# Performance work log

Measured on AMD Instinct MI355X. Metric: run time of the kernel, lower is better.

Reference implementation:

```python
import jax, jax.numpy as jnp
import numpy as np

N = 50000      # nodes per type
E = 800000     # edges per relation
D = 128        # input feature dim
H = 128        # hidden_channels


def setup_inputs() -> dict:
    key = jax.random.key(0)
    ks = jax.random.split(key, 20)
    f = lambda k, shp: jax.random.normal(k, shp, dtype=jnp.float32) * 0.05
    inp = {
        "x_ligand": jax.random.normal(ks[0], (N, D), dtype=jnp.float32),
        "x_protein": jax.random.normal(ks[1], (N, D), dtype=jnp.float32),
        "ei_lp": jax.random.randint(ks[2], (2, E), 0, N, dtype=jnp.int64),
        "ei_pp": jax.random.randint(ks[3], (2, E), 0, N, dtype=jnp.int64),
        "ei_ll": jax.random.randint(ks[4], (2, E), 0, N, dtype=jnp.int64),
        "Wl_lp": f(ks[5], (D, H)), "bl_lp": f(ks[6], (H,)), "Wr_lp": f(ks[7], (D, H)),
        "Wl_pp": f(ks[8], (D, H)), "bl_pp": f(ks[9], (H,)), "Wr_pp": f(ks[10], (D, H)),
        "Wl_ll": f(ks[11], (D, H)), "bl_ll": f(ks[12], (H,)), "Wr_ll": f(ks[13], (D, H)),
        "W_out": f(ks[14], (H, 1)), "b_out": f(ks[15], (1,)),
    }
    return inp


def _sage(x_src, x_dst, edge_index, Wl, bl, Wr):
    # PyG SAGEConv: mean-aggregate neighbor (src) features onto dst, then
    # out = lin_l(agg) + lin_r(x_dst)  (lin_l has bias, lin_r does not)
    src, dst = edge_index[0], edge_index[1]
    n_dst = x_dst.shape[0]
    msgs = x_src[src]                                      # [E, D] gather
    s = jax.ops.segment_sum(msgs, dst, num_segments=n_dst) # [N_dst, D]
    cnt = jax.ops.segment_sum(jnp.ones((edge_index.shape[1],), x_src.dtype),
                              dst, num_segments=n_dst)     # [N_dst]
    agg = s / jnp.maximum(cnt, 1.0)[:, None]               # mean, 0 if isolated
    return agg @ Wl + bl + x_dst @ Wr


def reference(x_ligand, x_protein, ei_lp, ei_pp, ei_ll,
              Wl_lp, bl_lp, Wr_lp, Wl_pp, bl_pp, Wr_pp,
              Wl_ll, bl_ll, Wr_ll, W_out, b_out):
    # HeteroConv: sum contributions per destination node type
    protein_out = (_sage(x_ligand, x_protein, ei_lp, Wl_lp, bl_lp, Wr_lp)
                   + _sage(x_protein, x_protein, ei_pp, Wl_pp, bl_pp, Wr_pp))
    ligand_out = _sage(x_ligand, x_ligand, ei_ll, Wl_ll, bl_ll, Wr_ll)
    # relu per node type; only ligand is used downstream
    lig = jax.nn.relu(ligand_out).mean(axis=0)             # [H]
    _ = jax.nn.relu(protein_out)                           # computed in original
    return lig @ W_out + b_out                             # [1]
```

## Files before the change

### kernel.cpp

```cpp
#include <hip/hip_runtime.h>
#include <hip/hip_bf16.h>

#define DIM 128
#define EPB 4096
#define NRBIN 1024
#define RCAP 1280

typedef __attribute__((ext_vector_type(8))) short bf16x8;
typedef __attribute__((ext_vector_type(4))) float f32x4;
typedef __attribute__((ext_vector_type(4))) short short4v;
typedef __attribute__((ext_vector_type(4))) int int4v;

__device__ inline unsigned short f2bf(float f) {
  union { float f; unsigned u; } v; v.f = f;
  return (unsigned short)((v.u + 0x7FFFu + ((v.u >> 16) & 1u)) >> 16);
}
__device__ inline float lo_f(unsigned u) {
  union { unsigned u; float f; } v; v.u = u << 16; return v.f;
}
__device__ inline float hi_f(unsigned u) {
  union { unsigned u; float f; } v; v.u = u & 0xFFFF0000u; return v.f;
}

__global__ __launch_bounds__(256) void prep_kernel(
    const float* __restrict__ x, short* __restrict__ A,
    const float* __restrict__ Wl, const float* __restrict__ Wr,
    short* __restrict__ Bpack, int nnodes, int mpad, int xb) {
  const int bid = blockIdx.x;
  if (bid < xb) {
    int t = bid * 256 + threadIdx.x;
    int node = t >> 5;
    if (node >= mpad) return;
    int c = (t & 31) * 4;
    short4v o = (short4v){0, 0, 0, 0};
    if (node < nnodes) {
      float4 v = *reinterpret_cast<const float4*>(x + (size_t)node * DIM + c);
      o.x = (short)f2bf(v.x); o.y = (short)f2bf(v.y);
      o.z = (short)f2bf(v.z); o.w = (short)f2bf(v.w);
    }
    *reinterpret_cast<short4v*>(A + (size_t)node * 256 + 128 + c) = o;
  } else {
    int t = (bid - xb) * 256 + threadIdx.x;
    if (t >= 4096) return;
    int lane = t & 63, nt = (t >> 6) & 7, ks = t >> 9;
    int c = nt * 16 + (lane & 15);
    int kb = ks * 32 + ((lane >> 4) << 3);
    bf16x8 o;
#pragma unroll
    for (int j = 0; j < 8; ++j) {
      int k = kb + j;
      float v = (k < DIM) ? Wl[k * DIM + c] : Wr[(k - DIM) * DIM + c];
      o[j] = (short)f2bf(v);
    }
    reinterpret_cast<bf16x8*>(Bpack)[(ks * 8 + nt) * 64 + lane] = o;
  }
}

__global__ __launch_bounds__(256) void partition_kernel(
    const int* __restrict__ ei, unsigned* __restrict__ chunkbuf,
    int* __restrict__ startsT, int* __restrict__ countsT, int E) {
  __shared__ unsigned uns[EPB];
  __shared__ unsigned srt[EPB];
  __shared__ int lhist[NRBIN];
  __shared__ int lstart[NRBIN];
  __shared__ int tsum[256];
  const int tid = threadIdx.x;
  const int chunk = blockIdx.x;
  const int base = chunk * EPB;
  const int count = min(EPB, E - base);

#pragma unroll
  for (int r = 0; r < NRBIN / 256; ++r) lhist[tid + 256 * r] = 0;
  __syncthreads();

  for (int r = 0; r < EPB / 1024; ++r) {
    int i = r * 1024 + tid * 4;
    if (i + 3 < count) {
      int4 s4 = *reinterpret_cast<const int4*>(ei + base + i);
      int4 d4 = *reinterpret_cast<const int4*>(ei + E + base + i);
      int ss[4] = {s4.x, s4.y, s4.z, s4.w};
      int dd[4] = {d4.x, d4.y, d4.z, d4.w};
#pragma unroll
      for (int k = 0; k < 4; ++k) {
        unsigned reg = (unsigned)dd[k] >> 6;
        uns[i + k] = (reg << 22) | ((unsigned)(dd[k] & 63) << 16) | (unsigned)ss[k];
        atomicAdd(&lhist[reg], 1);
      }
    } else {
      for (int k = 0; k < 4; ++k) {
        if (i + k < count) {
          int s = ei[base + i + k], d = ei[E + base + i + k];
          unsigned reg = (unsigned)d >> 6;
          uns[i + k] = (reg << 22) | ((unsigned)(d & 63) << 16) | (unsigned)s;
          atomicAdd(&lhist[reg], 1);
        }
      }
    }
  }
  __syncthreads();

  int h0 = lhist[tid * 4], h1 = lhist[tid * 4 + 1];
  int h2 = lhist[tid * 4 + 2], h3 = lhist[tid * 4 + 3];
  int local = h0 + h1 + h2 + h3;
  tsum[tid] = local;
  __syncthreads();
  for (int o = 1; o < 256; o <<= 1) {
    int t = (tid >= o) ? tsum[tid - o] : 0;
    __syncthreads();
    tsum[tid] += t;
    __syncthreads();
  }
  int tb = tsum[tid] - local;
  lstart[tid * 4]     = tb;
  lstart[tid * 4 + 1] = tb + h0;
  lstart[tid * 4 + 2] = tb + h0 + h1;
  lstart[tid * 4 + 3] = tb + h0 + h1 + h2;
  lhist[tid * 4] = 0; lhist[tid * 4 + 1] = 0;
  lhist[tid * 4 + 2] = 0; lhist[tid * 4 + 3] = 0;
  __syncthreads();

  for (int i = tid; i < count; i += 256) {
    unsigned e = uns[i];
    unsigned reg = e >> 22;
    int pos = lstart[reg] + atomicAdd(&lhist[reg], 1);
    srt[pos] = e;
  }
  __syncthreads();

  for (int r = 0; r < EPB / 1024; ++r) {
    int i = r * 1024 + tid * 4;
    if (i + 3 < count) {
      int4v v = {(int)srt[i], (int)srt[i + 1], (int)srt[i + 2], (int)srt[i + 3]};
      *reinterpret_cast<int4v*>(chunkbuf + (size_t)chunk * EPB + i) = v;
    } else {
      for (int k = 0; k < 4; ++k)
        if (i + k < count) chunkbuf[(size_t)chunk * EPB + i + k] = srt[i + k];
    }
  }
  for (int r = tid; r < NRBIN; r += 256) {
    startsT[(size_t)chunk * NRBIN + r] = lstart[r];
    countsT[(size_t)chunk * NRBIN + r] = lhist[r];
  }
}

__global__ __launch_bounds__(256) void compact_kernel(
    const unsigned* __restrict__ chunkbuf, const int* __restrict__ startsT,
    const int* __restrict__ countsT, int nchunk, unsigned* __restrict__ csr,
    int* __restrict__ cnt, int* __restrict__ off) {
  __shared__ unsigned raw[RCAP];
  __shared__ unsigned srt[RCAP];
  __shared__ int h[64];
  __shared__ int start[64];
  __shared__ int tsum[256];
  const int region = blockIdx.x;
  const int tid = threadIdx.x;

  int cn = 0, st = 0;
  if (tid < nchunk) {
    cn = countsT[(size_t)tid * NRBIN + region];
    st = startsT[(size_t)tid * NRBIN + region];
  }
  tsum[tid] = cn;
  __syncthreads();
  for (int o = 1; o < 256; o <<= 1) {
    int t = (tid >= o) ? tsum[tid - o] : 0;
    __syncthreads();
    tsum[tid] += t;
    __syncthreads();
  }
  const int pfx = tsum[tid] - cn;
  int total = min(tsum[255], RCAP);

  const unsigned* src = chunkbuf + (size_t)tid * EPB + st;
  for (int j = 0; j < cn && pfx + j < RCAP; ++j) raw[pfx + j] = src[j];
  if (tid < 64) h[tid] = 0;
  __syncthreads();

  for (int i = tid; i < total; i += 256) atomicAdd(&h[(raw[i] >> 16) & 63], 1);
  __syncthreads();
  if (tid == 0) {
    int s = 0;
    for (int i = 0; i < 64; ++i) { start[i] = s; s += h[i]; }
  }
  __syncthreads();
  if (tid < 64) {
    int node = region * 64 + tid;
    cnt[node] = h[tid];
    off[node] = region * RCAP + start[tid];
    h[tid] = 0;
  }
  __syncthreads();
  for (int i = tid; i < total; i += 256) {
    unsigned e = raw[i];
    int d = (e >> 16) & 63;
    int pos = start[d] + atomicAdd(&h[d], 1);
    srt[pos] = e & 0xFFFFu;
  }
  __syncthreads();
  for (int i = tid; i < total; i += 256) csr[(size_t)region * RCAP + i] = srt[i];
}

__global__ __launch_bounds__(256) void agg_kernel(
    const int* __restrict__ cnt, const int* __restrict__ off,
    const unsigned* __restrict__ bucket, short* __restrict__ A,
    int nnodes, int mpad) {
  const int wid = (blockIdx.x * 256 + threadIdx.x) >> 6;
  const int lane = threadIdx.x & 63;
  if (wid >= mpad) return;
  unsigned* dst = reinterpret_cast<unsigned*>(A + (size_t)wid * 256) + lane;
  if (wid >= nnodes) { *dst = 0u; return; }
  const int deg  = __builtin_amdgcn_readfirstlane(cnt[wid]);
  const int base = __builtin_amdgcn_readfirstlane(off[wid]);
  const unsigned* xs = reinterpret_cast<const unsigned*>(A) + 64 + lane;

  unsigned ent = (lane < deg) ? bucket[base + lane] : 0u;
  const int dcap = min(deg, 64);

  float l0 = 0.f, h0 = 0.f, l1 = 0.f, h1 = 0.f;
  int j = 0;
  for (; j + 7 < dcap; j += 8) {
    unsigned u[8];
#pragma unroll
    for (int k = 0; k < 8; ++k) {
      int s = __builtin_amdgcn_readlane((int)ent, j + k);
      u[k] = xs[(size_t)s * 128];
    }
#pragma unroll
    for (int k = 0; k < 8; ++k) {
      if (k & 1) { l1 += lo_f(u[k]); h1 += hi_f(u[k]); }
      else       { l0 += lo_f(u[k]); h0 += hi_f(u[k]); }
    }
  }
  for (; j < dcap; ++j) {
    int s = __builtin_amdgcn_readlane((int)ent, j);
    unsigned u0 = xs[(size_t)s * 128];
    l0 += lo_f(u0); h0 += hi_f(u0);
  }
  for (; j < deg; ++j) {
    int s = __builtin_amdgcn_readfirstlane((int)bucket[base + j]);
    unsigned u0 = xs[(size_t)s * 128];
    l0 += lo_f(u0); h0 += hi_f(u0);
  }
  const float r = 1.0f / fmaxf((float)deg, 1.0f);
  const float av = (l0 + l1) * r;
  const float bv = (h0 + h1) * r;
  *dst = (unsigned)f2bf(av) | ((unsigned)f2bf(bv) << 16);
}

__global__ __launch_bounds__(256) void mfma_kernel(
    const short* __restrict__ A, const short* __restrict__ Bpack,
    const float* __restrict__ bl, float* __restrict__ partial, int nnodes) {
  __shared__ short a_lds[64 * 256];
  const int tid = threadIdx.x;
  const int wave = tid >> 6, lane = tid & 63;
  const int mt = blockIdx.x;
  const size_t abase = (size_t)mt * 64 * 256;

#pragma unroll
  for (int r = 0; r < 8; ++r) {
    int i = tid + 256 * r;
    int row = i >> 5, kc = i & 31;
    bf16x8 v = *reinterpret_cast<const bf16x8*>(A + abase + row * 256 + kc * 8);
    int byte = (row * 512 + kc * 16) ^ ((row & 7) << 4);
    *reinterpret_cast<bf16x8*>(reinterpret_cast<char*>(a_lds) + byte) = v;
  }
  __syncthreads();

  f32x4 acc[8];
#pragma unroll
  for (int nt = 0; nt < 8; ++nt) acc[nt] = (f32x4){0.f, 0.f, 0.f, 0.f};

  const int arow = wave * 16 + (lane & 15);
  const int kgrp = lane >> 4;
  const bf16x8* Bp = reinterpret_cast<const bf16x8*>(Bpack);

#pragma unroll
  for (int ks = 0; ks < 8; ++ks) {
    int byte = (arow * 512 + (ks * 32 + kgrp * 8) * 2) ^ ((arow & 7) << 4);
    bf16x8 a = *reinterpret_cast<const bf16x8*>(reinterpret_cast<char*>(a_lds) + byte);
#pragma unroll
    for (int nt = 0; nt < 8; ++nt) {
      bf16x8 b = Bp[(ks * 8 + nt) * 64 + lane];
      acc[nt] = __builtin_amdgcn_mfma_f32_16x16x32_bf16(a, b, acc[nt], 0, 0, 0);
    }
  }

  const int col16 = lane & 15;
  const int rowbase = mt * 64 + wave * 16 + kgrp * 4;
#pragma unroll
  for (int nt = 0; nt < 8; ++nt) {
    const int c = nt * 16 + col16;
    const float bb = bl[c];
    float s = 0.f;
#pragma unroll
    for (int rg = 0; rg < 4; ++rg) {
      float v = fmaxf(acc[nt][rg] + bb, 0.f);
      s += (rowbase + rg < nnodes) ? v : 0.f;
    }
    s += __shfl_xor(s, 16);
    s += __shfl_xor(s, 32);
    if (kgrp == 0) partial[((size_t)mt * 4 + wave) * DIM + c] = s;
  }
}

__global__ __launch_bounds__(256) void red1_kernel(
    const float* __restrict__ partial, int nrows, float* __restrict__ red) {
  __shared__ float tmp[128];
  const int c = threadIdx.x & 127;
  const int half = threadIdx.x >> 7;
  const int chunk = (nrows + 127) / 128;
  const int r0 = blockIdx.x * chunk;
  const int r1 = min(r0 + chunk, nrows);
  float s = 0.f;
  for (int r = r0 + half; r < r1; r += 2) s += partial[(size_t)r * DIM + c];
  if (half) tmp[c] = s;
  __syncthreads();
  if (!half) red[(size_t)blockIdx.x * DIM + c] = s + tmp[c];
}

__global__ __launch_bounds__(256) void red2_kernel(
    const float* __restrict__ red, const float* __restrict__ Wout,
    const float* __restrict__ bout, float* __restrict__ out, int nnodes) {
  __shared__ float tmp[128];
  __shared__ float prod[128];
  const int c = threadIdx.x & 127;
  const int half = threadIdx.x >> 7;
  float s = 0.f;
  for (int r = half; r < 128; r += 2) s += red[(size_t)r * DIM + c];
  if (half) tmp[c] = s;
  __syncthreads();
  if (!half) prod[c] = (s + tmp[c]) * Wout[c];
  __syncthreads();
  if (threadIdx.x == 0) {
    float v = 0.f;
    for (int i = 0; i < 128; ++i) v += prod[i];
    out[0] = v / (float)nnodes + bout[0];
  }
}

extern "C" void kernel_launch(void* const* d_in, const int* in_sizes, int n_in,
                              void* d_out, int out_size, void* d_ws, size_t ws_size,
                              hipStream_t stream) {
  const float* x    = (const float*)d_in[0];
  const int*   ei   = (const int*)d_in[4];
  const float* Wl   = (const float*)d_in[11];
  const float* bl   = (const float*)d_in[12];
  const float* Wr   = (const float*)d_in[13];
  const float* Wout = (const float*)d_in[14];
  const float* bout = (const float*)d_in[15];

  const int nnodes = in_sizes[0] / DIM;
  const int E = in_sizes[4] / 2;
  const int mtiles = (nnodes + 63) / 64;
  const int mpad = mtiles * 64;
  const int nchunk = (E + EPB - 1) / EPB;

  unsigned* chunkbuf = (unsigned*)d_ws;
  int*      startsT  = (int*)(chunkbuf + (size_t)nchunk * EPB);
  int*      countsT  = startsT + (size_t)nchunk * NRBIN;
  unsigned* csr      = (unsigned*)(countsT + (size_t)nchunk * NRBIN);
  int*      cnt      = (int*)(csr + (size_t)mtiles * RCAP);
  int*      off      = cnt + mpad;
  short*    A        = (short*)(off + mpad);
  short*    Bpack    = A + (size_t)mpad * 256;
  float*    red      = (float*)(Bpack + 32768);
  float*    partial  = (float*)chunkbuf;

  const int xb = mpad / 8;
  prep_kernel<<<xb + 16, 256, 0, stream>>>(x, A, Wl, Wr, Bpack, nnodes, mpad, xb);

  partition_kernel<<<nchunk, 256, 0, stream>>>(ei, chunkbuf, startsT, countsT, E);

  compact_kernel<<<mtiles, 256, 0, stream>>>(chunkbuf, startsT, countsT, nchunk,
                                             csr, cnt, off);

  agg_kernel<<<(mpad + 3) / 4, 256, 0, stream>>>(cnt, off, csr, A, nnodes, mpad);

  mfma_kernel<<<mtiles, 256, 0, stream>>>(A, Bpack, bl, partial, nnodes);

  red1_kernel<<<128, 256, 0, stream>>>(partial, mtiles * 4, red);
  red2_kernel<<<1, 256, 0, stream>>>(red, Wout, bout, (float*)d_out, nnodes);
}
```

Before: 95.15 us.

## Fuse prep and partition kernels; unroll aggregation gather by 16

Merges the bf16 conversion/weight-packing kernel into the edge partition kernel as extra blocks, removing one launch and letting both run concurrently. The aggregation kernel gets a 16-wide unrolled gather loop to keep more loads in flight, plus a launch-bounds occupancy hint. The trade-off is that prep blocks now carry the partition kernel's large shared-memory allocation, which may limit how many of them fit on a CU at once.

```diff
diff --git a/kernel.cpp b/kernel.cpp
--- a/kernel.cpp
+++ b/kernel.cpp
@@ -22,50 +22,52 @@
   union { unsigned u; float f; } v; v.u = u & 0xFFFF0000u; return v.f;
 }
 
-__global__ __launch_bounds__(256) void prep_kernel(
+__global__ __launch_bounds__(256) void prep_part_kernel(
+    const int* __restrict__ ei, unsigned* __restrict__ chunkbuf,
+    int* __restrict__ startsT, int* __restrict__ countsT, int E, int nchunk,
     const float* __restrict__ x, short* __restrict__ A,
     const float* __restrict__ Wl, const float* __restrict__ Wr,
     short* __restrict__ Bpack, int nnodes, int mpad, int xb) {
-  const int bid = blockIdx.x;
-  if (bid < xb) {
-    int t = bid * 256 + threadIdx.x;
-    int node = t >> 5;
-    if (node >= mpad) return;
-    int c = (t & 31) * 4;
-    short4v o = (short4v){0, 0, 0, 0};
-    if (node < nnodes) {
-      float4 v = *reinterpret_cast<const float4*>(x + (size_t)node * DIM + c);
-      o.x = (short)f2bf(v.x); o.y = (short)f2bf(v.y);
-      o.z = (short)f2bf(v.z); o.w = (short)f2bf(v.w);
-    }
-    *reinterpret_cast<short4v*>(A + (size_t)node * 256 + 128 + c) = o;
-  } else {
-    int t = (bid - xb) * 256 + threadIdx.x;
-    if (t >= 4096) return;
-    int lane = t & 63, nt = (t >> 6) & 7, ks = t >> 9;
-    int c = nt * 16 + (lane & 15);
-    int kb = ks * 32 + ((lane >> 4) << 3);
-    bf16x8 o;
-#pragma unroll
-    for (int j = 0; j < 8; ++j) {
-      int k = kb + j;
-      float v = (k < DIM) ? Wl[k * DIM + c] : Wr[(k - DIM) * DIM + c];
-      o[j] = (short)f2bf(v);
-    }
-    reinterpret_cast<bf16x8*>(Bpack)[(ks * 8 + nt) * 64 + lane] = o;
-  }
-}
-
-__global__ __launch_bounds__(256) void partition_kernel(
-    const int* __restrict__ ei, unsigned* __restrict__ chunkbuf,
-    int* __restrict__ startsT, int* __restrict__ countsT, int E) {
   __shared__ unsigned uns[EPB];
   __shared__ unsigned srt[EPB];
   __shared__ int lhist[NRBIN];
   __shared__ int lstart[NRBIN];
   __shared__ int tsum[256];
   const int tid = threadIdx.x;
-  const int chunk = blockIdx.x;
+  const int bid = blockIdx.x;
+
+  if (bid >= nchunk) {
+    if (bid < nchunk + xb) {
+      int t = (bid - nchunk) * 256 + tid;
+      int node = t >> 5;
+      if (node >= mpad) return;
+      int c = (t & 31) * 4;
+      short4v o = (short4v){0, 0, 0, 0};
+      if (node < nnodes) {
+        float4 v = *reinterpret_cast<const float4*>(x + (size_t)node * DIM + c);
+        o.x = (short)f2bf(v.x); o.y = (short)f2bf(v.y);
+        o.z = (short)f2bf(v.z); o.w = (short)f2bf(v.w);
+      }
+      *reinterpret_cast<short4v*>(A + (size_t)node * 256 + 128 + c) = o;
+    } else {
+      int t = (bid - nchunk - xb) * 256 + tid;
+      if (t >= 4096) return;
+      int lane = t & 63, nt = (t >> 6) & 7, ks = t >> 9;
+      int c = nt * 16 + (lane & 15);
+      int kb = ks * 32 + ((lane >> 4) << 3);
+      bf16x8 o;
+#pragma unroll
+      for (int j = 0; j < 8; ++j) {
+        int k = kb + j;
+        float v = (k < DIM) ? Wl[k * DIM + c] : Wr[(k - DIM) * DIM + c];
+        o[j] = (short)f2bf(v);
+      }
+      reinterpret_cast<bf16x8*>(Bpack)[(ks * 8 + nt) * 64 + lane] = o;
+    }
+    return;
+  }
+
+  const int chunk = bid;
   const int base = chunk * EPB;
   const int count = min(EPB, E - base);
 
@@ -200,7 +202,7 @@
   for (int i = tid; i < total; i += 256) csr[(size_t)region * RCAP + i] = srt[i];
 }
 
-__global__ __launch_bounds__(256) void agg_kernel(
+__global__ __launch_bounds__(256, 4) void agg_kernel(
     const int* __restrict__ cnt, const int* __restrict__ off,
     const unsigned* __restrict__ bucket, short* __restrict__ A,
     int nnodes, int mpad) {
@@ -218,6 +220,19 @@
 
   float l0 = 0.f, h0 = 0.f, l1 = 0.f, h1 = 0.f;
   int j = 0;
+  for (; j + 15 < dcap; j += 16) {
+    unsigned u[16];
+#pragma unroll
+    for (int k = 0; k < 16; ++k) {
+      int s = __builtin_amdgcn_readlane((int)ent, j + k);
+      u[k] = xs[(size_t)s * 128];
+    }
+#pragma unroll
+    for (int k = 0; k < 16; ++k) {
+      if (k & 1) { l1 += lo_f(u[k]); h1 += hi_f(u[k]); }
+      else       { l0 += lo_f(u[k]); h0 += hi_f(u[k]); }
+    }
+  }
   for (; j + 7 < dcap; j += 8) {
     unsigned u[8];
 #pragma unroll
@@ -367,9 +382,9 @@
   float*    partial  = (float*)chunkbuf;
 
   const int xb = mpad / 8;
-  prep_kernel<<<xb + 16, 256, 0, stream>>>(x, A, Wl, Wr, Bpack, nnodes, mpad, xb);
-
-  partition_kernel<<<nchunk, 256, 0, stream>>>(ei, chunkbuf, startsT, countsT, E);
+  prep_part_kernel<<<nchunk + xb + 16, 256, 0, stream>>>(
+      ei, chunkbuf, startsT, countsT, E, nchunk,
+      x, A, Wl, Wr, Bpack, nnodes, mpad, xb);
 
   compact_kernel<<<mtiles, 256, 0, stream>>>(chunkbuf, startsT, countsT, nchunk,
                                              csr, cnt, off);
```

New measurement: 91.11 us (median of 2 runs). -4.3%, faster.
